# Optimization experiments

Hardware: AMD Instinct MI355X
Metric: run time of the kernel (lower is better)

The kernel has to match this reference:

```python
import jax, jax.numpy as jnp
import numpy as np

B = 16384
D = 4096  # d_mlp == d_hidden in this module
K = 64


def setup_inputs() -> dict:
    key = jax.random.key(0)
    k1, k2, k3, k4 = jax.random.split(key, 4)
    x = jax.random.normal(k1, (B, D), dtype=jnp.float32)
    ema_frequency_counter = jax.random.uniform(k2, (D,), dtype=jnp.float32)
    W_enc = jax.random.normal(k3, (D, D), dtype=jnp.float32)
    # W_dec initialized like the module: randn, then scaled by 0.1/(norm+2*eps-ish);
    # the exact init scaling: norm over dim=1, norm += eps(=1), then *= 0.1/(norm+eps)
    W_dec_raw = jax.random.normal(k4, (D, D), dtype=jnp.float32)
    eps = 1.0
    norm = jnp.linalg.norm(W_dec_raw, axis=1, keepdims=True) + eps
    W_dec = W_dec_raw * (0.1 / (norm + eps))
    pre_bias = jnp.zeros((D,), dtype=jnp.float32)
    latent_bias = jnp.zeros((D,), dtype=jnp.float32)
    return {
        'x': x,
        'ema_frequency_counter': ema_frequency_counter,
        'W_enc': W_enc,
        'W_dec': W_dec,
        'pre_bias': pre_bias,
        'latent_bias': latent_bias,
        'k': K,
    }


def topk_activation(acts, k):
    # torch.topk -> ReLU on values -> scatter back into zeros
    vals, idx = jax.lax.top_k(acts, k)          # [B, k]
    vals = jax.nn.relu(vals)
    rows = jnp.arange(acts.shape[0])[:, None]   # [B, 1]
    return jnp.zeros_like(acts).at[rows, idx].set(vals)


def reference(x, ema_frequency_counter, W_enc, W_dec, pre_bias, latent_bias, k):
    # method='reconstruct' path of TopKAutoEncoder.forward
    x_center = x - pre_bias                     # [B, D]
    acts = x_center @ W_enc + latent_bias       # [B, D]
    acts_top_k = topk_activation(acts, k)       # sparse (k nonzeros/row)
    x_reconstruct = acts_top_k @ W_dec + pre_bias
    return x_reconstruct
```

## Files before the change

### kernel.cpp

```cpp
#include <hip/hip_runtime.h>
#include <hip/hip_bf16.h>
#include <stdint.h>


typedef _Float16 half8 __attribute__((ext_vector_type(8)));
typedef float f32x4 __attribute__((ext_vector_type(4)));
typedef unsigned short ushort8 __attribute__((ext_vector_type(8)));

#define B_ROWS 16384
#define D_DIM  4096
#define TOPK   64
#define MARGIN 0.25f
#define NTILES (D_DIM / 32)

__device__ __forceinline__ void gload_lds16(const void* g, void* l) {
  __builtin_amdgcn_global_load_lds(
      (const __attribute__((address_space(1))) unsigned int*)g,
      (__attribute__((address_space(3))) unsigned int*)l, 16, 0, 0);
}

__device__ __forceinline__ unsigned short f2bf(float f) {
  unsigned u = __float_as_uint(f);
  unsigned r = (u + 0x7fffu + ((u >> 16) & 1u)) >> 16;
  return (unsigned short)r;
}


__global__ __launch_bounds__(256) void conv_x(
    const float* __restrict__ x, const float* __restrict__ pre_bias,
    _Float16* __restrict__ Xh) {
  size_t g = ((size_t)blockIdx.x * 256 + threadIdx.x) * 8;
  int col = (int)(g & (D_DIM - 1));
  float4 a = *(const float4*)(x + g);
  float4 b = *(const float4*)(x + g + 4);
  float4 p = *(const float4*)(pre_bias + col);
  float4 q = *(const float4*)(pre_bias + col + 4);
  half8 h;
  h[0] = (_Float16)(a.x - p.x); h[1] = (_Float16)(a.y - p.y);
  h[2] = (_Float16)(a.z - p.z); h[3] = (_Float16)(a.w - p.w);
  h[4] = (_Float16)(b.x - q.x); h[5] = (_Float16)(b.y - q.y);
  h[6] = (_Float16)(b.z - q.z); h[7] = (_Float16)(b.w - q.w);
  *(half8*)(Xh + g) = h;
}

__global__ __launch_bounds__(256) void transp_w(
    const float* __restrict__ W, _Float16* __restrict__ WhT,
    float* __restrict__ WT) {
  __shared__ float tile[64][65];
  int bx = blockIdx.x, by = blockIdx.y;
  int tx = threadIdx.x & 63, ty4 = threadIdx.x >> 6;
  #pragma unroll 4
  for (int i = 0; i < 16; ++i) {
    int r = ty4 * 16 + i;
    tile[r][tx] = W[(size_t)(by * 64 + r) * D_DIM + bx * 64 + tx];
  }
  __syncthreads();
  #pragma unroll 4
  for (int i = 0; i < 16; ++i) {
    int r = ty4 * 16 + i;
    float v = tile[tx][r];
    size_t o = (size_t)(bx * 64 + r) * D_DIM + by * 64 + tx;
    WT[o] = v;
    WhT[o] = (_Float16)v;
  }
}

__global__ __launch_bounds__(256) void conv_wd(
    const float* __restrict__ W, unsigned short* __restrict__ o) {
  size_t g = ((size_t)blockIdx.x * 256 + threadIdx.x) * 8;
  float4 a = *(const float4*)(W + g);
  float4 b = *(const float4*)(W + g + 4);
  ushort8 v;
  v[0] = f2bf(a.x); v[1] = f2bf(a.y); v[2] = f2bf(a.z); v[3] = f2bf(a.w);
  v[4] = f2bf(b.x); v[5] = f2bf(b.y); v[6] = f2bf(b.z); v[7] = f2bf(b.w);
  *(ushort8*)(o + g) = v;
}


#define TILE_BODY(T, VMSTR)                                                    \
  do {                                                                         \
    asm volatile("s_waitcnt " VMSTR ::: "memory");                             \
    __builtin_amdgcn_s_barrier();                                              \
    asm volatile("" ::: "memory");                                             \
    const int tt3 = (T) + 3;                                                   \
    if (tt3 < NTILES) {                                                        \
      const int bo = (tt3 & 3) * 8192;                                         \
      const int kk = tt3 * 32;                                                 \
      gload_lds16(aSrc0 + kk, AsB + bo + dst0);                                \
      gload_lds16(aSrc1 + kk, AsB + bo + dst1);                                \
    }                                                                          \
    {                                                                          \
      const int ab = ((T) & 3) * 8192;                                         \
      half8 bf[4], af[4];                                                      \
      _Pragma("unroll") for (int nj = 0; nj < 4; ++nj)                         \
          bf[nj] = *(const half8*)(BsB + ab + bBase + nj * 512);               \
      _Pragma("unroll") for (int mi = 0; mi < 4; ++mi)                         \
          af[mi] = *(const half8*)(AsB + ab + aBase + mi * 512);               \
      __builtin_amdgcn_s_setprio(1);                                           \
      _Pragma("unroll") for (int mi = 0; mi < 4; ++mi)                         \
          _Pragma("unroll") for (int nj = 0; nj < 4; ++nj)                     \
          acc[mi][nj] = __builtin_amdgcn_mfma_f32_16x16x32_f16(                \
              af[mi], bf[nj], acc[mi][nj], 0, 0, 0);                           \
      __builtin_amdgcn_s_setprio(0);                                           \
      if (tt3 < NTILES) {                                                      \
        const int bo = (tt3 & 3) * 8192;                                       \
        const int kk = tt3 * 32;                                               \
        gload_lds16(bSrc0 + kk, BsB + bo + dst0);                              \
        gload_lds16(bSrc1 + kk, BsB + bo + dst1);                              \
      }                                                                        \
      _Pragma("unroll") for (int mi = 0; mi < 4; ++mi)                         \
          af[mi] = *(const half8*)(AsB + ab + aBase + (mi + 4) * 512);         \
      __builtin_amdgcn_s_setprio(1);                                           \
      _Pragma("unroll") for (int mi = 0; mi < 4; ++mi)                         \
          _Pragma("unroll") for (int nj = 0; nj < 4; ++nj)                     \
          acc[mi + 4][nj] = __builtin_amdgcn_mfma_f32_16x16x32_f16(            \
              af2[mi], bf[nj], acc[mi + 4][nj], 0, 0, 0);                      \
      __builtin_amdgcn_s_setprio(0);                                           \
    }                                                                          \
  } while (0)

#undef TILE_BODY
#define TILE_BODY(T, VMSTR)                                                    \
  do {                                                                         \
    asm volatile("s_waitcnt " VMSTR ::: "memory");                             \
    __builtin_amdgcn_s_barrier();                                              \
    asm volatile("" ::: "memory");                                             \
    const int tt3 = (T) + 3;                                                   \
    if (tt3 < NTILES) {                                                        \
      const int bo = (tt3 & 3) * 8192;                                         \
      const int kk = tt3 * 32;                                                 \
      gload_lds16(aSrc0 + kk, AsB + bo + dst0);                                \
      gload_lds16(aSrc1 + kk, AsB + bo + dst1);                                \
    }                                                                          \
    {                                                                          \
      const int ab = ((T) & 3) * 8192;                                         \
      half8 bf[4], af[4];                                                      \
      _Pragma("unroll") for (int nj = 0; nj < 4; ++nj)                         \
          bf[nj] = *(const half8*)(BsB + ab + bBase + nj * 512);               \
      _Pragma("unroll") for (int mi = 0; mi < 4; ++mi)                         \
          af[mi] = *(const half8*)(AsB + ab + aBase + mi * 512);               \
      __builtin_amdgcn_s_setprio(1);                                           \
      _Pragma("unroll") for (int mi = 0; mi < 4; ++mi)                         \
          _Pragma("unroll") for (int nj = 0; nj < 4; ++nj)                     \
          acc[mi][nj] = __builtin_amdgcn_mfma_f32_16x16x32_f16(                \
              af[mi], bf[nj], acc[mi][nj], 0, 0, 0);                           \
      __builtin_amdgcn_s_setprio(0);                                           \
      if (tt3 < NTILES) {                                                      \
        const int bo = (tt3 & 3) * 8192;                                       \
        const int kk = tt3 * 32;                                               \
        gload_lds16(bSrc0 + kk, BsB + bo + dst0);                              \
        gload_lds16(bSrc1 + kk, BsB + bo + dst1);                              \
      }                                                                        \
      _Pragma("unroll") for (int mi = 0; mi < 4; ++mi)                         \
          af[mi] = *(const half8*)(AsB + ab + aBase + (mi + 4) * 512);         \
      __builtin_amdgcn_s_setprio(1);                                           \
      _Pragma("unroll") for (int mi = 0; mi < 4; ++mi)                         \
          _Pragma("unroll") for (int nj = 0; nj < 4; ++nj)                     \
          acc[mi + 4][nj] = __builtin_amdgcn_mfma_f32_16x16x32_f16(            \
              af[mi], bf[nj], acc[mi + 4][nj], 0, 0, 0);                       \
      __builtin_amdgcn_s_setprio(0);                                           \
    }                                                                          \
  } while (0)

__global__ __launch_bounds__(512, 2) void gemm_f16(
    const _Float16* __restrict__ A, const _Float16* __restrict__ Bt,
    const float* __restrict__ latent_bias, float* __restrict__ C) {
  extern __shared__ _Float16 ldsbuf[];
  _Float16* AsB = ldsbuf;
  _Float16* BsB = ldsbuf + 4 * 8192;

  const int tid = threadIdx.x;
  const int lane = tid & 63, wave = tid >> 6;
  const int wr = wave >> 2, wc = wave & 3;

  int bid = blockIdx.x;
  int swz = (bid & 7) * (1024 >> 3) + (bid >> 3);
  const int bmBase = (swz >> 4) * 256;
  const int bnBase = (swz & 15) * 256;

  const int i0 = tid, i1 = 512 + tid;
  const int s0 = i0 ^ ((i0 >> 3) & 3), s1 = i1 ^ ((i1 >> 3) & 3);
  const _Float16* aSrc0 = A + (size_t)(bmBase + (s0 >> 2)) * D_DIM + (s0 & 3) * 8;
  const _Float16* aSrc1 = A + (size_t)(bmBase + (s1 >> 2)) * D_DIM + (s1 & 3) * 8;
  const _Float16* bSrc0 = Bt + (size_t)(bnBase + (s0 >> 2)) * D_DIM + (s0 & 3) * 8;
  const _Float16* bSrc1 = Bt + (size_t)(bnBase + (s1 >> 2)) * D_DIM + (s1 & 3) * 8;
  const int dst0 = i0 * 8, dst1 = i1 * 8;

  const int fr = lane & 15, c4 = lane >> 4;
  const int swzc = (c4 ^ ((fr >> 1) & 3)) * 8;
  const int aBase = (wr * 128 + fr) * 32 + swzc;
  const int bBase = (wc * 64 + fr) * 32 + swzc;

  f32x4 acc[8][4];
  #pragma unroll
  for (int i = 0; i < 8; ++i)
    #pragma unroll
    for (int j = 0; j < 4; ++j) acc[i][j] = f32x4{0.f, 0.f, 0.f, 0.f};

  #pragma unroll
  for (int tt = 0; tt < 3; ++tt) {
    const int bo = tt * 8192, kk = tt * 32;
    gload_lds16(aSrc0 + kk, AsB + bo + dst0);
    gload_lds16(aSrc1 + kk, AsB + bo + dst1);
    gload_lds16(bSrc0 + kk, BsB + bo + dst0);
    gload_lds16(bSrc1 + kk, BsB + bo + dst1);
  }

  for (int t = 0; t < NTILES - 2; ++t) TILE_BODY(t, "vmcnt(8)");
  TILE_BODY(NTILES - 2, "vmcnt(4)");
  TILE_BODY(NTILES - 1, "vmcnt(0)");

  const int crow0 = bmBase + wr * 128 + c4 * 4;
  const int ccol0 = bnBase + wc * 64 + fr;
  #pragma unroll
  for (int mi = 0; mi < 8; ++mi)
    #pragma unroll
    for (int nj = 0; nj < 4; ++nj) {
      int col = ccol0 + nj * 16;
      float lb = latent_bias[col];
      #pragma unroll
      for (int r = 0; r < 4; ++r)
        C[(size_t)(crow0 + mi * 16 + r) * D_DIM + col] = acc[mi][nj][r] + lb;
    }
}


__global__ __launch_bounds__(256) void topk_classify(
    const float* __restrict__ acts, float* __restrict__ vals,
    int* __restrict__ idxs, int* __restrict__ ambIdx,
    int* __restrict__ rowMeta) {
  const int row = blockIdx.x;
  const int tid = threadIdx.x;
  const int lane = tid & 63, wave = tid >> 6;
  __shared__ int hist[4096];
  __shared__ int sred[8];
  const float* arow = acts + (size_t)row * D_DIM;
  float fv[16];
  #pragma unroll
  for (int i = 0; i < 4; ++i) {
    float4 a = *(const float4*)(arow + i * 1024 + tid * 4);
    fv[4 * i + 0] = a.x; fv[4 * i + 1] = a.y;
    fv[4 * i + 2] = a.z; fv[4 * i + 3] = a.w;
  }
  #pragma unroll
  for (int i = 0; i < 16; ++i) hist[tid * 16 + i] = 0;
  __syncthreads();
  #pragma unroll
  for (int e = 0; e < 16; ++e) {
    int b = (int)((fv[e] + 512.0f) * 4.0f);
    b = b < 0 ? 0 : (b > 4095 ? 4095 : b);
    atomicAdd(&hist[b], 1);
  }
  __syncthreads();
  int loc[16];
  int s = 0;
  #pragma unroll
  for (int i = 15; i >= 0; --i) { s += hist[tid * 16 + i]; loc[i] = s; }
  int x = s;
  #pragma unroll
  for (int off = 1; off < 64; off <<= 1) {
    int y = __shfl_down(x, off);
    if (lane + off < 64) x += y;
  }
  if (lane == 0) sred[wave] = x;
  __syncthreads();
  int after = 0;
  for (int w = wave + 1; w < 4; ++w) after += sred[w];
  const int sufAfter = (x - s) + after;
  int cand = -1;
  #pragma unroll
  for (int i = 0; i < 16; ++i)
    if (loc[i] + sufAfter >= TOPK) cand = tid * 16 + i;
  #pragma unroll
  for (int off = 32; off; off >>= 1) {
    int y = __shfl_down(cand, off);
    cand = y > cand ? y : cand;
  }
  if (lane == 0) sred[4 + wave] = cand;
  __syncthreads();
  int b0 = sred[4] > sred[5] ? sred[4] : sred[5];
  int b1 = sred[6] > sred[7] ? sred[6] : sred[7];
  const int bstar = b0 > b1 ? b0 : b1;
  const float Tlo = (bstar == 0) ? -1e30f : (bstar * 0.25f - 512.0f);
  const float Thi = (bstar >= 4095) ? 1e30f : ((bstar + 1) * 0.25f - 512.0f);
  const float vhi = Thi + MARGIN;
  const float vlo = Tlo - MARGIN;
  int mC = 0, aC = 0;
  #pragma unroll
  for (int i = 0; i < 16; ++i) {
    float v = fv[i];
    if (v > vhi) ++mC;
    else if (v >= vlo) ++aC;
  }
  int xs = mC | (aC << 16);
  #pragma unroll
  for (int off = 1; off < 64; off <<= 1) {
    int y = __shfl_up(xs, off);
    if (lane >= off) xs += y;
  }
  if (lane == 63) sred[wave] = xs;
  __syncthreads();
  int base = 0;
  for (int w = 0; w < 4; ++w)
    if (w < wave) base += sred[w];
  int tot = sred[0] + sred[1] + sred[2] + sred[3];
  int incl = base + xs;
  int mp = (incl & 0xffff) - mC;
  int ap = (incl >> 16) - aC;
  int mTot = tot & 0xffff, aTot = tot >> 16;
  const int need = TOPK - mTot;
  const bool fast = (aTot == need);
  #pragma unroll
  for (int e = 0; e < 16; ++e) {
    float v = fv[e];
    int d = (e >> 2) * 1024 + tid * 4 + (e & 3);
    if (v > vhi) {
      vals[(size_t)row * TOPK + mp] = fmaxf(v, 0.0f);
      idxs[(size_t)row * TOPK + mp] = d;
      ++mp;
    } else if (v >= vlo) {
      if (fast) {
        vals[(size_t)row * TOPK + mTot + ap] = fmaxf(v, 0.0f);
        idxs[(size_t)row * TOPK + mTot + ap] = d;
      } else if (ap < 128) {
        ambIdx[(size_t)row * 128 + ap] = d;
      }
      ++ap;
    }
  }
  if (tid == 0) {
    rowMeta[row * 2 + 0] = mTot;
    rowMeta[row * 2 + 1] = (fast || need <= 0) ? 0 : ((aTot > 128) ? 128 : aTot);
  }
}


__global__ __launch_bounds__(256) void rescue(
    const float* __restrict__ x, const float* __restrict__ WT,
    const float* __restrict__ pre_bias, const float* __restrict__ latent_bias,
    const float* __restrict__ acts, const int* __restrict__ ambIdx,
    const int* __restrict__ rowMeta, float* __restrict__ vals,
    int* __restrict__ idxs) {
  const int row = blockIdx.x;
  const int m = rowMeta[row * 2 + 0];
  const int s = rowMeta[row * 2 + 1];
  const int need = TOPK - m;
  const int tid = threadIdx.x;
  if (need <= 0 || s <= 0) return;
  if (s == need) {
    if (tid < s) {
      int d = ambIdx[(size_t)row * 128 + tid];
      float v = acts[(size_t)row * D_DIM + d];
      vals[(size_t)row * TOPK + m + tid] = fmaxf(v, 0.0f);
      idxs[(size_t)row * TOPK + m + tid] = d;
    }
    return;
  }
  __shared__ double exv[128];
  const int lane = tid & 63, wave = tid >> 6;
  const float* xr = x + (size_t)row * D_DIM;
  for (int c = wave; c < s; c += 4) {
    int d = ambIdx[(size_t)row * 128 + c];
    const float* wrow = WT + (size_t)d * D_DIM;
    double acc = 0.0;
    #pragma unroll 4
    for (int t = 0; t < 16; ++t) {
      int k0 = t * 256 + lane * 4;
      float4 xv = *(const float4*)(xr + k0);
      float4 pv = *(const float4*)(pre_bias + k0);
      float4 wv = *(const float4*)(wrow + k0);
      acc = fma((double)xv.x - (double)pv.x, (double)wv.x, acc);
      acc = fma((double)xv.y - (double)pv.y, (double)wv.y, acc);
      acc = fma((double)xv.z - (double)pv.z, (double)wv.z, acc);
      acc = fma((double)xv.w - (double)pv.w, (double)wv.w, acc);
    }
    #pragma unroll
    for (int off = 32; off; off >>= 1) acc += __shfl_down(acc, off);
    if (lane == 0) exv[c] = acc + (double)latent_bias[d];
  }
  __syncthreads();
  if (tid == 0) {
    for (int t = 0; t < need; ++t) {
      double best = -1.0e300; int besti = 1 << 30; int bestc = -1;
      for (int c = 0; c < s; ++c) {
        double v = exv[c];
        int d = ambIdx[(size_t)row * 128 + c];
        if (v > best || (v == best && d < besti)) {
          best = v; besti = d; bestc = c;
        }
      }
      vals[(size_t)row * TOPK + m + t] = fmaxf((float)best, 0.0f);
      idxs[(size_t)row * TOPK + m + t] = besti;
      exv[bestc] = -1.0e300;
    }
  }
}


__global__ __launch_bounds__(256) void reconstruct(
    const unsigned short* __restrict__ Wd, const float* __restrict__ vals,
    const int* __restrict__ idxs, const float* __restrict__ pre_bias,
    float* __restrict__ out) {
  const int bid = blockIdx.x;
  const int cb = bid & 7, rowblk = bid >> 3;
  const int tid = threadIdx.x, lane = tid & 63, wave = tid >> 6;
  const int row = rowblk * 4 + wave;
  const int col0 = cb * 512 + lane * 8;
  __shared__ float sval[256];
  __shared__ int sidx[256];
  sval[tid] = vals[(size_t)(rowblk * 4 + (tid >> 6)) * TOPK + (tid & 63)];
  sidx[tid] = idxs[(size_t)(rowblk * 4 + (tid >> 6)) * TOPK + (tid & 63)];
  __syncthreads();
  float acc[8];
  float4 p0 = *(const float4*)(pre_bias + col0);
  float4 p1 = *(const float4*)(pre_bias + col0 + 4);
  acc[0] = p0.x; acc[1] = p0.y; acc[2] = p0.z; acc[3] = p0.w;
  acc[4] = p1.x; acc[5] = p1.y; acc[6] = p1.z; acc[7] = p1.w;
  #pragma unroll 4
  for (int k = 0; k < TOPK; ++k) {
    float v = sval[wave * 64 + k];
    int d = sidx[wave * 64 + k];
    ushort8 w = *(const ushort8*)(Wd + (size_t)d * D_DIM + col0);
    #pragma unroll
    for (int j = 0; j < 8; ++j)
      acc[j] = fmaf(v, __uint_as_float(((unsigned)w[j]) << 16), acc[j]);
  }
  float4 o0 = {acc[0], acc[1], acc[2], acc[3]};
  float4 o1 = {acc[4], acc[5], acc[6], acc[7]};
  *(float4*)(out + (size_t)row * D_DIM + col0) = o0;
  *(float4*)(out + (size_t)row * D_DIM + col0 + 4) = o1;
}


extern "C" void kernel_launch(void* const* d_in, const int* in_sizes, int n_in,
                              void* d_out, int out_size, void* d_ws,
                              size_t ws_size, hipStream_t stream) {
  const float* x           = (const float*)d_in[0];
  const float* W_enc       = (const float*)d_in[2];
  const float* W_dec       = (const float*)d_in[3];
  const float* pre_bias    = (const float*)d_in[4];
  const float* latent_bias = (const float*)d_in[5];
  float* out = (float*)d_out;
  char* ws = (char*)d_ws;
  size_t off = 0;
  auto alloc = [&](size_t bytes) {
    size_t o = off;
    off = (off + bytes + 255) & ~(size_t)255;
    return o;
  };
  _Float16* Xh        = (_Float16*)(ws + alloc((size_t)B_ROWS * D_DIM * 2));
  _Float16* WhT       = (_Float16*)(ws + alloc((size_t)D_DIM * D_DIM * 2));
  float* WT           = (float*)(ws + alloc((size_t)D_DIM * D_DIM * 4));
  unsigned short* Wd  = (unsigned short*)(ws + alloc((size_t)D_DIM * D_DIM * 2));
  float* vals         = (float*)(ws + alloc((size_t)B_ROWS * TOPK * 4));
  int* idxs           = (int*)(ws + alloc((size_t)B_ROWS * TOPK * 4));
  int* ambIdx         = (int*)(ws + alloc((size_t)B_ROWS * 128 * 4));
  int* rowMeta        = (int*)(ws + alloc((size_t)B_ROWS * 2 * 4));
  (void)ws_size; (void)in_sizes; (void)n_in; (void)out_size;

  (void)hipFuncSetAttribute((const void*)gemm_f16,
                            hipFuncAttributeMaxDynamicSharedMemorySize,
                            131072);

  conv_x<<<(B_ROWS * D_DIM / 8) / 256, 256, 0, stream>>>(x, pre_bias, Xh);
  transp_w<<<dim3(D_DIM / 64, D_DIM / 64), 256, 0, stream>>>(W_enc, WhT, WT);
  conv_wd<<<((size_t)D_DIM * D_DIM / 8) / 256, 256, 0, stream>>>(W_dec, Wd);
  gemm_f16<<<(B_ROWS / 256) * (D_DIM / 256), 512, 131072, stream>>>(
      Xh, WhT, latent_bias, out);
  topk_classify<<<B_ROWS, 256, 0, stream>>>(out, vals, idxs, ambIdx, rowMeta);
  rescue<<<B_ROWS, 256, 0, stream>>>(x, WT, pre_bias, latent_bias, out,
                                     ambIdx, rowMeta, vals, idxs);
  reconstruct<<<(B_ROWS / 4) * 8, 256, 0, stream>>>(Wd, vals, idxs, pre_bias,
                                                    out);
}
```

Before: 1.158 ms.

## Fuse top-k classify and fp64 rescue into one kernel with finer histogram

Merges the top-k classification and rescue kernels into one per-row kernel that keeps ambiguous candidate indices in shared memory instead of global workspace. This removes a kernel launch and the global round trip for candidate indices and row metadata. It also doubles histogram resolution to 8192 bins and narrows the ambiguity margin, so fewer candidates need exact fp64 recomputation. The cost is higher LDS use per block, which may lower occupancy, and a tighter margin that relies on the fp16 GEMM error staying within it.

```diff
diff --git a/kernel.cpp b/kernel.cpp
--- a/kernel.cpp
+++ b/kernel.cpp
@@ -10,7 +10,7 @@
 #define B_ROWS 16384
 #define D_DIM  4096
 #define TOPK   64
-#define MARGIN 0.25f
+#define MARGIN 0.1875f
 #define NTILES (D_DIM / 32)
 
 __device__ __forceinline__ void gload_lds16(const void* g, void* l) {
@@ -77,49 +77,6 @@
 }
 
 
-#define TILE_BODY(T, VMSTR)                                                    \
-  do {                                                                         \
-    asm volatile("s_waitcnt " VMSTR ::: "memory");                             \
-    __builtin_amdgcn_s_barrier();                                              \
-    asm volatile("" ::: "memory");                                             \
-    const int tt3 = (T) + 3;                                                   \
-    if (tt3 < NTILES) {                                                        \
-      const int bo = (tt3 & 3) * 8192;                                         \
-      const int kk = tt3 * 32;                                                 \
-      gload_lds16(aSrc0 + kk, AsB + bo + dst0);                                \
-      gload_lds16(aSrc1 + kk, AsB + bo + dst1);                                \
-    }                                                                          \
-    {                                                                          \
-      const int ab = ((T) & 3) * 8192;                                         \
-      half8 bf[4], af[4];                                                      \
-      _Pragma("unroll") for (int nj = 0; nj < 4; ++nj)                         \
-          bf[nj] = *(const half8*)(BsB + ab + bBase + nj * 512);               \
-      _Pragma("unroll") for (int mi = 0; mi < 4; ++mi)                         \
-          af[mi] = *(const half8*)(AsB + ab + aBase + mi * 512);               \
-      __builtin_amdgcn_s_setprio(1);                                           \
-      _Pragma("unroll") for (int mi = 0; mi < 4; ++mi)                         \
-          _Pragma("unroll") for (int nj = 0; nj < 4; ++nj)                     \
-          acc[mi][nj] = __builtin_amdgcn_mfma_f32_16x16x32_f16(                \
-              af[mi], bf[nj], acc[mi][nj], 0, 0, 0);                           \
-      __builtin_amdgcn_s_setprio(0);                                           \
-      if (tt3 < NTILES) {                                                      \
-        const int bo = (tt3 & 3) * 8192;                                       \
-        const int kk = tt3 * 32;                                               \
-        gload_lds16(bSrc0 + kk, BsB + bo + dst0);                              \
-        gload_lds16(bSrc1 + kk, BsB + bo + dst1);                              \
-      }                                                                        \
-      _Pragma("unroll") for (int mi = 0; mi < 4; ++mi)                         \
-          af[mi] = *(const half8*)(AsB + ab + aBase + (mi + 4) * 512);         \
-      __builtin_amdgcn_s_setprio(1);                                           \
-      _Pragma("unroll") for (int mi = 0; mi < 4; ++mi)                         \
-          _Pragma("unroll") for (int nj = 0; nj < 4; ++nj)                     \
-          acc[mi + 4][nj] = __builtin_amdgcn_mfma_f32_16x16x32_f16(            \
-              af2[mi], bf[nj], acc[mi + 4][nj], 0, 0, 0);                      \
-      __builtin_amdgcn_s_setprio(0);                                           \
-    }                                                                          \
-  } while (0)
-
-#undef TILE_BODY
 #define TILE_BODY(T, VMSTR)                                                    \
   do {                                                                         \
     asm volatile("s_waitcnt " VMSTR ::: "memory");                             \
@@ -225,15 +182,18 @@
 }
 
 
-__global__ __launch_bounds__(256) void topk_classify(
-    const float* __restrict__ acts, float* __restrict__ vals,
-    int* __restrict__ idxs, int* __restrict__ ambIdx,
-    int* __restrict__ rowMeta) {
+__global__ __launch_bounds__(256) void topk_full(
+    const float* __restrict__ acts, const float* __restrict__ x,
+    const float* __restrict__ WT, const float* __restrict__ pre_bias,
+    const float* __restrict__ latent_bias, float* __restrict__ vals,
+    int* __restrict__ idxs) {
   const int row = blockIdx.x;
   const int tid = threadIdx.x;
   const int lane = tid & 63, wave = tid >> 6;
-  __shared__ int hist[4096];
+  __shared__ int hist[8192];
   __shared__ int sred[8];
+  __shared__ int ambL[128];
+  __shared__ double exv[128];
   const float* arow = acts + (size_t)row * D_DIM;
   float fv[16];
   #pragma unroll
@@ -243,34 +203,34 @@
     fv[4 * i + 2] = a.z; fv[4 * i + 3] = a.w;
   }
   #pragma unroll
-  for (int i = 0; i < 16; ++i) hist[tid * 16 + i] = 0;
+  for (int i = 0; i < 32; ++i) hist[tid * 32 + i] = 0;
   __syncthreads();
   #pragma unroll
   for (int e = 0; e < 16; ++e) {
-    int b = (int)((fv[e] + 512.0f) * 4.0f);
-    b = b < 0 ? 0 : (b > 4095 ? 4095 : b);
+    int b = (int)((fv[e] + 512.0f) * 8.0f);
+    b = b < 0 ? 0 : (b > 8191 ? 8191 : b);
     atomicAdd(&hist[b], 1);
   }
   __syncthreads();
-  int loc[16];
+  int loc[32];
   int s = 0;
   #pragma unroll
-  for (int i = 15; i >= 0; --i) { s += hist[tid * 16 + i]; loc[i] = s; }
-  int x = s;
+  for (int i = 31; i >= 0; --i) { s += hist[tid * 32 + i]; loc[i] = s; }
+  int xw = s;
   #pragma unroll
   for (int off = 1; off < 64; off <<= 1) {
-    int y = __shfl_down(x, off);
-    if (lane + off < 64) x += y;
-  }
-  if (lane == 0) sred[wave] = x;
+    int y = __shfl_down(xw, off);
+    if (lane + off < 64) xw += y;
+  }
+  if (lane == 0) sred[wave] = xw;
   __syncthreads();
   int after = 0;
   for (int w = wave + 1; w < 4; ++w) after += sred[w];
-  const int sufAfter = (x - s) + after;
+  const int sufAfter = (xw - s) + after;
   int cand = -1;
   #pragma unroll
-  for (int i = 0; i < 16; ++i)
-    if (loc[i] + sufAfter >= TOPK) cand = tid * 16 + i;
+  for (int i = 0; i < 32; ++i)
+    if (loc[i] + sufAfter >= TOPK) cand = tid * 32 + i;
   #pragma unroll
   for (int off = 32; off; off >>= 1) {
     int y = __shfl_down(cand, off);
@@ -281,8 +241,8 @@
   int b0 = sred[4] > sred[5] ? sred[4] : sred[5];
   int b1 = sred[6] > sred[7] ? sred[6] : sred[7];
   const int bstar = b0 > b1 ? b0 : b1;
-  const float Tlo = (bstar == 0) ? -1e30f : (bstar * 0.25f - 512.0f);
-  const float Thi = (bstar >= 4095) ? 1e30f : ((bstar + 1) * 0.25f - 512.0f);
+  const float Tlo = (bstar == 0) ? -1e30f : (bstar * 0.125f - 512.0f);
+  const float Thi = (bstar >= 8191) ? 1e30f : ((bstar + 1) * 0.125f - 512.0f);
   const float vhi = Thi + MARGIN;
   const float vlo = Tlo - MARGIN;
   int mC = 0, aC = 0;
@@ -323,44 +283,18 @@
         vals[(size_t)row * TOPK + mTot + ap] = fmaxf(v, 0.0f);
         idxs[(size_t)row * TOPK + mTot + ap] = d;
       } else if (ap < 128) {
-        ambIdx[(size_t)row * 128 + ap] = d;
+        ambL[ap] = d;
       }
       ++ap;
     }
   }
-  if (tid == 0) {
-    rowMeta[row * 2 + 0] = mTot;
-    rowMeta[row * 2 + 1] = (fast || need <= 0) ? 0 : ((aTot > 128) ? 128 : aTot);
-  }
-}
-
-
-__global__ __launch_bounds__(256) void rescue(
-    const float* __restrict__ x, const float* __restrict__ WT,
-    const float* __restrict__ pre_bias, const float* __restrict__ latent_bias,
-    const float* __restrict__ acts, const int* __restrict__ ambIdx,
-    const int* __restrict__ rowMeta, float* __restrict__ vals,
-    int* __restrict__ idxs) {
-  const int row = blockIdx.x;
-  const int m = rowMeta[row * 2 + 0];
-  const int s = rowMeta[row * 2 + 1];
-  const int need = TOPK - m;
-  const int tid = threadIdx.x;
-  if (need <= 0 || s <= 0) return;
-  if (s == need) {
-    if (tid < s) {
-      int d = ambIdx[(size_t)row * 128 + tid];
-      float v = acts[(size_t)row * D_DIM + d];
-      vals[(size_t)row * TOPK + m + tid] = fmaxf(v, 0.0f);
-      idxs[(size_t)row * TOPK + m + tid] = d;
-    }
-    return;
-  }
-  __shared__ double exv[128];
-  const int lane = tid & 63, wave = tid >> 6;
+  if (fast) return;
+
+  __syncthreads();
+  const int sN = aTot > 128 ? 128 : aTot;
   const float* xr = x + (size_t)row * D_DIM;
-  for (int c = wave; c < s; c += 4) {
-    int d = ambIdx[(size_t)row * 128 + c];
+  for (int c = wave; c < sN; c += 4) {
+    int d = ambL[c];
     const float* wrow = WT + (size_t)d * D_DIM;
     double acc = 0.0;
     #pragma unroll 4
@@ -382,15 +316,15 @@
   if (tid == 0) {
     for (int t = 0; t < need; ++t) {
       double best = -1.0e300; int besti = 1 << 30; int bestc = -1;
-      for (int c = 0; c < s; ++c) {
+      for (int c = 0; c < sN; ++c) {
         double v = exv[c];
-        int d = ambIdx[(size_t)row * 128 + c];
+        int d = ambL[c];
         if (v > best || (v == best && d < besti)) {
           best = v; besti = d; bestc = c;
         }
       }
-      vals[(size_t)row * TOPK + m + t] = fmaxf((float)best, 0.0f);
-      idxs[(size_t)row * TOPK + m + t] = besti;
+      vals[(size_t)row * TOPK + mTot + t] = fmaxf((float)best, 0.0f);
+      idxs[(size_t)row * TOPK + mTot + t] = besti;
       exv[bestc] = -1.0e300;
     }
   }
@@ -454,8 +388,6 @@
   unsigned short* Wd  = (unsigned short*)(ws + alloc((size_t)D_DIM * D_DIM * 2));
   float* vals         = (float*)(ws + alloc((size_t)B_ROWS * TOPK * 4));
   int* idxs           = (int*)(ws + alloc((size_t)B_ROWS * TOPK * 4));
-  int* ambIdx         = (int*)(ws + alloc((size_t)B_ROWS * 128 * 4));
-  int* rowMeta        = (int*)(ws + alloc((size_t)B_ROWS * 2 * 4));
   (void)ws_size; (void)in_sizes; (void)n_in; (void)out_size;
 
   (void)hipFuncSetAttribute((const void*)gemm_f16,
@@ -467,9 +399,8 @@
   conv_wd<<<((size_t)D_DIM * D_DIM / 8) / 256, 256, 0, stream>>>(W_dec, Wd);
   gemm_f16<<<(B_ROWS / 256) * (D_DIM / 256), 512, 131072, stream>>>(
       Xh, WhT, latent_bias, out);
-  topk_classify<<<B_ROWS, 256, 0, stream>>>(out, vals, idxs, ambIdx, rowMeta);
-  rescue<<<B_ROWS, 256, 0, stream>>>(x, WT, pre_bias, latent_bias, out,
-                                     ambIdx, rowMeta, vals, idxs);
+  topk_full<<<B_ROWS, 256, 0, stream>>>(out, x, WT, pre_bias, latent_bias,
+                                        vals, idxs);
   reconstruct<<<(B_ROWS / 4) * 8, 256, 0, stream>>>(Wd, vals, idxs, pre_bias,
                                                     out);
 }
```

Measured after the change: 1.169 ms. About the same (+1.0%).

## Use 1024-thread GEMM blocks with 64x64 per-wave tiles

Applied to the files above, without the earlier changes.

The f16 encoder GEMM block grows from 8 to 16 waves, so each wave now owns a 64x64 output sub-tile instead of 128x64. Each thread issues one A and one B global-to-LDS load per stage instead of two each, and the vmcnt waits are halved to match. Halving the accumulator array cuts register pressure and puts more waves behind each barrier to hide latency. In exchange each wave re-reads B fragments from LDS more often relative to its MFMA work, and 1024-thread barriers cost more.

```diff
diff --git a/kernel.cpp b/kernel.cpp
--- a/kernel.cpp
+++ b/kernel.cpp
@@ -86,8 +86,8 @@
     if (tt3 < NTILES) {                                                        \
       const int bo = (tt3 & 3) * 8192;                                         \
       const int kk = tt3 * 32;                                                 \
-      gload_lds16(aSrc0 + kk, AsB + bo + dst0);                                \
-      gload_lds16(aSrc1 + kk, AsB + bo + dst1);                                \
+      gload_lds16(aSrc + kk, AsB + bo + dstL);                                 \
+      gload_lds16(bSrc + kk, BsB + bo + dstL);                                 \
     }                                                                          \
     {                                                                          \
       const int ab = ((T) & 3) * 8192;                                         \
@@ -102,67 +102,10 @@
           acc[mi][nj] = __builtin_amdgcn_mfma_f32_16x16x32_f16(                \
               af[mi], bf[nj], acc[mi][nj], 0, 0, 0);                           \
       __builtin_amdgcn_s_setprio(0);                                           \
-      if (tt3 < NTILES) {                                                      \
-        const int bo = (tt3 & 3) * 8192;                                       \
-        const int kk = tt3 * 32;                                               \
-        gload_lds16(bSrc0 + kk, BsB + bo + dst0);                              \
-        gload_lds16(bSrc1 + kk, BsB + bo + dst1);                              \
-      }                                                                        \
-      _Pragma("unroll") for (int mi = 0; mi < 4; ++mi)                         \
-          af[mi] = *(const half8*)(AsB + ab + aBase + (mi + 4) * 512);         \
-      __builtin_amdgcn_s_setprio(1);                                           \
-      _Pragma("unroll") for (int mi = 0; mi < 4; ++mi)                         \
-          _Pragma("unroll") for (int nj = 0; nj < 4; ++nj)                     \
-          acc[mi + 4][nj] = __builtin_amdgcn_mfma_f32_16x16x32_f16(            \
-              af2[mi], bf[nj], acc[mi + 4][nj], 0, 0, 0);                      \
-      __builtin_amdgcn_s_setprio(0);                                           \
     }                                                                          \
   } while (0)
 
-#undef TILE_BODY
-#define TILE_BODY(T, VMSTR)                                                    \
-  do {                                                                         \
-    asm volatile("s_waitcnt " VMSTR ::: "memory");                             \
-    __builtin_amdgcn_s_barrier();                                              \
-    asm volatile("" ::: "memory");                                             \
-    const int tt3 = (T) + 3;                                                   \
-    if (tt3 < NTILES) {                                                        \
-      const int bo = (tt3 & 3) * 8192;                                         \
-      const int kk = tt3 * 32;                                                 \
-      gload_lds16(aSrc0 + kk, AsB + bo + dst0);                                \
-      gload_lds16(aSrc1 + kk, AsB + bo + dst1);                                \
-    }                                                                          \
-    {                                                                          \
-      const int ab = ((T) & 3) * 8192;                                         \
-      half8 bf[4], af[4];                                                      \
-      _Pragma("unroll") for (int nj = 0; nj < 4; ++nj)                         \
-          bf[nj] = *(const half8*)(BsB + ab + bBase + nj * 512);               \
-      _Pragma("unroll") for (int mi = 0; mi < 4; ++mi)                         \
-          af[mi] = *(const half8*)(AsB + ab + aBase + mi * 512);               \
-      __builtin_amdgcn_s_setprio(1);                                           \
-      _Pragma("unroll") for (int mi = 0; mi < 4; ++mi)                         \
-          _Pragma("unroll") for (int nj = 0; nj < 4; ++nj)                     \
-          acc[mi][nj] = __builtin_amdgcn_mfma_f32_16x16x32_f16(                \
-              af[mi], bf[nj], acc[mi][nj], 0, 0, 0);                           \
-      __builtin_amdgcn_s_setprio(0);                                           \
-      if (tt3 < NTILES) {                                                      \
-        const int bo = (tt3 & 3) * 8192;                                       \
-        const int kk = tt3 * 32;                                               \
-        gload_lds16(bSrc0 + kk, BsB + bo + dst0);                              \
-        gload_lds16(bSrc1 + kk, BsB + bo + dst1);                              \
-      }                                                                        \
-      _Pragma("unroll") for (int mi = 0; mi < 4; ++mi)                         \
-          af[mi] = *(const half8*)(AsB + ab + aBase + (mi + 4) * 512);         \
-      __builtin_amdgcn_s_setprio(1);                                           \
-      _Pragma("unroll") for (int mi = 0; mi < 4; ++mi)                         \
-          _Pragma("unroll") for (int nj = 0; nj < 4; ++nj)                     \
-          acc[mi + 4][nj] = __builtin_amdgcn_mfma_f32_16x16x32_f16(            \
-              af[mi], bf[nj], acc[mi + 4][nj], 0, 0, 0);                       \
-      __builtin_amdgcn_s_setprio(0);                                           \
-    }                                                                          \
-  } while (0)
-
-__global__ __launch_bounds__(512, 2) void gemm_f16(
+__global__ __launch_bounds__(1024, 4) void gemm_f16(
     const _Float16* __restrict__ A, const _Float16* __restrict__ Bt,
     const float* __restrict__ latent_bias, float* __restrict__ C) {
   extern __shared__ _Float16 ldsbuf[];
@@ -171,49 +114,44 @@
 
   const int tid = threadIdx.x;
   const int lane = tid & 63, wave = tid >> 6;
-  const int wr = wave >> 2, wc = wave & 3;
+  const int wm = wave >> 2, wn = wave & 3;
 
   int bid = blockIdx.x;
   int swz = (bid & 7) * (1024 >> 3) + (bid >> 3);
   const int bmBase = (swz >> 4) * 256;
   const int bnBase = (swz & 15) * 256;
 
-  const int i0 = tid, i1 = 512 + tid;
-  const int s0 = i0 ^ ((i0 >> 3) & 3), s1 = i1 ^ ((i1 >> 3) & 3);
-  const _Float16* aSrc0 = A + (size_t)(bmBase + (s0 >> 2)) * D_DIM + (s0 & 3) * 8;
-  const _Float16* aSrc1 = A + (size_t)(bmBase + (s1 >> 2)) * D_DIM + (s1 & 3) * 8;
-  const _Float16* bSrc0 = Bt + (size_t)(bnBase + (s0 >> 2)) * D_DIM + (s0 & 3) * 8;
-  const _Float16* bSrc1 = Bt + (size_t)(bnBase + (s1 >> 2)) * D_DIM + (s1 & 3) * 8;
-  const int dst0 = i0 * 8, dst1 = i1 * 8;
+  const int s = tid ^ ((tid >> 3) & 3);
+  const _Float16* aSrc = A + (size_t)(bmBase + (s >> 2)) * D_DIM + (s & 3) * 8;
+  const _Float16* bSrc = Bt + (size_t)(bnBase + (s >> 2)) * D_DIM + (s & 3) * 8;
+  const int dstL = tid * 8;
 
   const int fr = lane & 15, c4 = lane >> 4;
   const int swzc = (c4 ^ ((fr >> 1) & 3)) * 8;
-  const int aBase = (wr * 128 + fr) * 32 + swzc;
-  const int bBase = (wc * 64 + fr) * 32 + swzc;
-
-  f32x4 acc[8][4];
-  #pragma unroll
-  for (int i = 0; i < 8; ++i)
+  const int aBase = (wm * 64 + fr) * 32 + swzc;
+  const int bBase = (wn * 64 + fr) * 32 + swzc;
+
+  f32x4 acc[4][4];
+  #pragma unroll
+  for (int i = 0; i < 4; ++i)
     #pragma unroll
     for (int j = 0; j < 4; ++j) acc[i][j] = f32x4{0.f, 0.f, 0.f, 0.f};
 
   #pragma unroll
   for (int tt = 0; tt < 3; ++tt) {
     const int bo = tt * 8192, kk = tt * 32;
-    gload_lds16(aSrc0 + kk, AsB + bo + dst0);
-    gload_lds16(aSrc1 + kk, AsB + bo + dst1);
-    gload_lds16(bSrc0 + kk, BsB + bo + dst0);
-    gload_lds16(bSrc1 + kk, BsB + bo + dst1);
-  }
-
-  for (int t = 0; t < NTILES - 2; ++t) TILE_BODY(t, "vmcnt(8)");
-  TILE_BODY(NTILES - 2, "vmcnt(4)");
+    gload_lds16(aSrc + kk, AsB + bo + dstL);
+    gload_lds16(bSrc + kk, BsB + bo + dstL);
+  }
+
+  for (int t = 0; t < NTILES - 2; ++t) TILE_BODY(t, "vmcnt(4)");
+  TILE_BODY(NTILES - 2, "vmcnt(2)");
   TILE_BODY(NTILES - 1, "vmcnt(0)");
 
-  const int crow0 = bmBase + wr * 128 + c4 * 4;
-  const int ccol0 = bnBase + wc * 64 + fr;
-  #pragma unroll
-  for (int mi = 0; mi < 8; ++mi)
+  const int crow0 = bmBase + wm * 64 + c4 * 4;
+  const int ccol0 = bnBase + wn * 64 + fr;
+  #pragma unroll
+  for (int mi = 0; mi < 4; ++mi)
     #pragma unroll
     for (int nj = 0; nj < 4; ++nj) {
       int col = ccol0 + nj * 16;
@@ -465,7 +403,7 @@
   conv_x<<<(B_ROWS * D_DIM / 8) / 256, 256, 0, stream>>>(x, pre_bias, Xh);
   transp_w<<<dim3(D_DIM / 64, D_DIM / 64), 256, 0, stream>>>(W_enc, WhT, WT);
   conv_wd<<<((size_t)D_DIM * D_DIM / 8) / 256, 256, 0, stream>>>(W_dec, Wd);
-  gemm_f16<<<(B_ROWS / 256) * (D_DIM / 256), 512, 131072, stream>>>(
+  gemm_f16<<<(B_ROWS / 256) * (D_DIM / 256), 1024, 131072, stream>>>(
       Xh, WhT, latent_bias, out);
   topk_classify<<<B_ROWS, 256, 0, stream>>>(out, vals, idxs, ambIdx, rowMeta);
   rescue<<<B_ROWS, 256, 0, stream>>>(x, WT, pre_bias, latent_bias, out,
```

Measured after the change: 1.155 ms. No clear change (-0.3%).
